# Kernel tuning notes

Measured on AMD Instinct MI355X. Metric: run time of the kernel, lower is better.

## Reference

```python
import jax, jax.numpy as jnp
import numpy as np

B = 8192
LOD = 60      # latent_obs_dim
LSD = 2 * LOD # latent state dim
AD = 10       # act_dim
NB = 15       # num_basis
BW = 3        # bandwidth
H = 60        # control-net hidden units


def elup1(x):
    # exp(x) if x < 0 else x + 1 (positive covariance activation)
    return jnp.where(x < 0.0, jnp.exp(x), x + 1.0)


def setup_inputs() -> dict:
    key = jax.random.key(0)
    ks = jax.random.split(key, 16)
    inp = {
        "post_mean": jax.random.normal(ks[0], (B, LSD), jnp.float32),
        "cu": jax.random.uniform(ks[1], (B, LOD), jnp.float32) + 0.1,
        "cl": jax.random.uniform(ks[2], (B, LOD), jnp.float32) + 0.1,
        "cs": 0.01 * jax.random.normal(ks[3], (B, LOD), jnp.float32),
        "action": jax.random.normal(ks[4], (B, AD), jnp.float32),
        # transition basis matrices (params); original init is zeros/+-0.2*I,
        # use small random values for a non-degenerate numerical test
        "tm11": 0.05 * jax.random.normal(ks[5], (NB, LOD, LOD), jnp.float32),
        "tm12": 0.2 * jnp.eye(LOD)[None] + 0.02 * jax.random.normal(ks[6], (NB, LOD, LOD), jnp.float32),
        "tm21": -0.2 * jnp.eye(LOD)[None] + 0.02 * jax.random.normal(ks[7], (NB, LOD, LOD), jnp.float32),
        "tm22": 0.05 * jax.random.normal(ks[8], (NB, LOD, LOD), jnp.float32),
        # log transition noise, init elup1_inv(1.0) = 0.0 -> perturb slightly
        "log_noise": 0.1 * jax.random.normal(ks[9], (1, LSD), jnp.float32),
        # coefficient net: Linear(LSD -> NB) + Softmax (no hidden layers)
        "w_coef": jax.random.normal(ks[10], (NB, LSD), jnp.float32) / np.sqrt(LSD),
        "b_coef": jnp.zeros((NB,), jnp.float32),
        # control net: Linear(AD -> H) + ReLU + Linear(H -> LSD)
        "w_c1": jax.random.normal(ks[11], (H, AD), jnp.float32) / np.sqrt(AD),
        "b_c1": jnp.zeros((H,), jnp.float32),
        "w_c2": jax.random.normal(ks[12], (LSD, H), jnp.float32) / np.sqrt(H),
        "b_c2": jnp.zeros((LSD,), jnp.float32),
    }
    return inp


def _band_mask():
    idx = jnp.arange(LOD)
    return (jnp.abs(idx[:, None] - idx[None, :]) <= BW).astype(jnp.float32)


def reference(post_mean, cu, cl, cs, action,
              tm11, tm12, tm21, tm22, log_noise,
              w_coef, b_coef, w_c1, b_c1, w_c2, b_c2):
    mask = _band_mask()            # [LOD, LOD]
    eye = jnp.eye(LOD, dtype=post_mean.dtype)

    # coefficient net + softmax -> basis-weighted transition matrices
    coef = jax.nn.softmax(post_mean @ w_coef.T + b_coef, axis=-1)  # [B, NB]

    def mix(tm):  # [B, LOD, LOD], band-masked
        return jnp.einsum('bk,kij->bij', coef, tm) * mask

    t11 = mix(tm11) + eye
    t12 = mix(tm12)
    t21 = mix(tm21)
    t22 = mix(tm22) + eye

    # control net contribution
    control = jax.nn.relu(action @ w_c1.T + b_c1) @ w_c2.T + b_c2  # [B, LSD]

    trans_cov = elup1(log_noise)        # [1, LSD]
    tc_u = trans_cov[..., :LOD]
    tc_l = trans_cov[..., LOD:]

    mu = post_mean[:, :LOD]
    ml = post_mean[:, LOD:]

    bmv = lambda m, v: jnp.einsum('bij,bj->bi', m, v)

    nmu = bmv(t11, mu) + bmv(t12, ml)
    nml = bmv(t21, mu) + bmv(t22, ml)

    # diagonal covariance predict (dadat / dadbt)
    ncu = bmv(t11 ** 2, cu) + 2.0 * bmv(t11 * t12, cs) + bmv(t12 ** 2, cl) + tc_u
    ncl = bmv(t21 ** 2, cu) + 2.0 * bmv(t21 * t22, cs) + bmv(t22 ** 2, cl) + tc_l
    ncs = bmv(t21 * t11, cu) + bmv(t22 * t11, cs) + bmv(t21 * t12, cs) + bmv(t22 * t12, cl)

    next_mean = jnp.concatenate([nmu, nml], axis=-1) + control
    return (next_mean, ncu, ncl, ncs)
```

## Files before the change

kernel.cpp:

```cpp
#include <hip/hip_runtime.h>
#include <math.h>

#define BATCH 8192
#define LOD 60
#define LSD 120
#define AD 10
#define NB 15
#define BW 3
#define H 60

#define NM_SZ (BATCH * LSD)
#define NC_SZ (BATCH * LOD)

#define RGS 8
#define RG_ROWS 8
#define NJJ 16
#define VSJ 65
#define VSV (NJJ * VSJ)
#define PACK_FLOATS (RG_ROWS * NB * 28)
#define VS_OFF PACK_FLOATS
#define VS_FLOATS (5 * VSV)
#define OVL_FLOATS (VS_OFF + VS_FLOATS)
#define COEF_OFF VS_OFF
#define HID_OFF (VS_OFF + NB * 64)
#define OST_PLANE (RG_ROWS * 65)

typedef float v2f __attribute__((ext_vector_type(2)));
#define FMA2(a, b, c) __builtin_elementwise_fma((a), (b), (c))

__device__ __forceinline__ float elup1f(float x) {
    return x < 0.0f ? __expf(x) : x + 1.0f;
}

__global__ __launch_bounds__(256, 4) void k_fused(
    const float* __restrict__ pm, const float* __restrict__ cu,
    const float* __restrict__ cl, const float* __restrict__ cs,
    const float* __restrict__ action,
    const float* __restrict__ tm11, const float* __restrict__ tm12,
    const float* __restrict__ tm21, const float* __restrict__ tm22,
    const float* __restrict__ log_noise,
    const float* __restrict__ w_coef, const float* __restrict__ b_coef,
    const float* __restrict__ w_c1, const float* __restrict__ b_c1,
    const float* __restrict__ w_c2, const float* __restrict__ b_c2,
    float* __restrict__ out)
{
    __shared__ __align__(16) float ovl[OVL_FLOATS];

    const int tid  = threadIdx.x;
    const int lane = tid & 63;
    const int wv   = __builtin_amdgcn_readfirstlane(tid >> 6);

    const int bid  = blockIdx.x;
    const int xcd  = bid & 7;
    const int slot = bid >> 3;
    const int bg   = xcd * 16 + (slot >> 3);
    const int rg   = slot & 7;
    const int b0   = bg * 64;
    const int i0   = rg * RG_ROWS;

    float* pack_s = ovl;
    float* vsb    = ovl + VS_OFF;
    float* coefL  = ovl + COEF_OFF;
    float* hid_s  = ovl + HID_OFF;

    {
        const int k0 = wv, k1 = wv + 4, k2 = wv + 8;
        const int k3 = (wv < 3) ? wv + 12 : 14;
        const float4* pmv = (const float4*)(pm + (size_t)(b0 + lane) * LSD);
        const float4* w0 = (const float4*)(w_coef + k0 * LSD);
        const float4* w1 = (const float4*)(w_coef + k1 * LSD);
        const float4* w2 = (const float4*)(w_coef + k2 * LSD);
        const float4* w3 = (const float4*)(w_coef + k3 * LSD);
        v2f a0 = {0.f, 0.f}, a1 = {0.f, 0.f}, a2 = {0.f, 0.f}, a3 = {0.f, 0.f};
        #pragma unroll 6
        for (int d = 0; d < LSD / 4; ++d) {
            float4 p = pmv[d];
            v2f plo = {p.x, p.y}, phi = {p.z, p.w};
            float4 u0 = w0[d], u1 = w1[d], u2 = w2[d], u3 = w3[d];
            a0 = FMA2(plo, ((v2f){u0.x, u0.y}), a0);
            a0 = FMA2(phi, ((v2f){u0.z, u0.w}), a0);
            a1 = FMA2(plo, ((v2f){u1.x, u1.y}), a1);
            a1 = FMA2(phi, ((v2f){u1.z, u1.w}), a1);
            a2 = FMA2(plo, ((v2f){u2.x, u2.y}), a2);
            a2 = FMA2(phi, ((v2f){u2.z, u2.w}), a2);
            a3 = FMA2(plo, ((v2f){u3.x, u3.y}), a3);
            a3 = FMA2(phi, ((v2f){u3.z, u3.w}), a3);
        }
        coefL[k0 * 64 + lane] = a0.x + a0.y + b_coef[k0];
        coefL[k1 * 64 + lane] = a1.x + a1.y + b_coef[k1];
        coefL[k2 * 64 + lane] = a2.x + a2.y + b_coef[k2];
        if (wv < 3) coefL[k3 * 64 + lane] = a3.x + a3.y + b_coef[k3];
    }
    {
        v2f av2[5];
        const float2* a2p = (const float2*)(action + (size_t)(b0 + lane) * AD);
        #pragma unroll
        for (int z = 0; z < 5; ++z) { float2 t2 = a2p[z]; av2[z] = (v2f){t2.x, t2.y}; }
        #pragma unroll
        for (int q = 0; q < 15; ++q) {
            int h = wv * 15 + q;
            v2f acc2 = {0.f, 0.f};
            #pragma unroll
            for (int z = 0; z < 5; ++z)
                acc2 = FMA2(av2[z], *(const v2f*)(w_c1 + h * AD + 2 * z), acc2);
            float acc = acc2.x + acc2.y + b_c1[h];
            hid_s[h * 65 + lane] = fmaxf(acc, 0.0f);
        }
    }
    __syncthreads();

    float vr[20];
    {
        const int jj  = tid & 15;
        const int j   = i0 - BW + jj;
        const bool jok = (j >= 0) && (j < LOD);
        #pragma unroll
        for (int z = 0; z < 20; ++z) {
            const int idx = z * 256 + tid;
            const int blc = (idx >> 4) & 63;
            const int bb  = b0 + blc;
            float val = 0.0f;
            if (jok) {
                const int v = z >> 2;
                if (v == 0)      val = pm[bb * LSD + j];
                else if (v == 1) val = pm[bb * LSD + LOD + j];
                else if (v == 2) val = cu[bb * LOD + j];
                else if (v == 3) val = cl[bb * LOD + j];
                else             val = cs[bb * LOD + j];
            }
            vr[z] = val;
        }
    }

    for (int idx = tid; idx < PACK_FLOATS; idx += 256) {
        int m  = idx & 3;
        int q  = idx >> 2;
        int jo = q % 7;
        int q2 = q / 7;
        int k  = q2 % NB;
        int ri = q2 / NB;
        int i  = i0 + ri;
        int j  = i - BW + jo;
        const float* tmm = (m == 0) ? tm11 : (m == 1) ? tm12 : (m == 2) ? tm21 : tm22;
        float val = (i < LOD && j >= 0 && j < LOD) ? tmm[k * (LOD * LOD) + i * LOD + j] : 0.0f;
        pack_s[idx] = val;
    }

    float cf[NB];
    {
        float mx = -1e30f;
        #pragma unroll
        for (int k = 0; k < NB; ++k) { cf[k] = coefL[k * 64 + lane]; mx = fmaxf(mx, cf[k]); }
        float sm = 0.0f;
        #pragma unroll
        for (int k = 0; k < NB; ++k) { cf[k] = __expf(cf[k] - mx); sm += cf[k]; }
        float inv = 1.0f / sm;
        #pragma unroll
        for (int k = 0; k < NB; ++k) cf[k] *= inv;
    }

    const int r0g = i0 + 2 * wv;
    const int c0  = (r0g < LOD) ? r0g : LOD - 1;
    const int c1  = (r0g + 1 < LOD) ? r0g + 1 : LOD - 1;
    float ctl0 = b_c2[c0], ctl1 = b_c2[c1];
    float ctl2 = b_c2[LOD + c0], ctl3 = b_c2[LOD + c1];
    #pragma unroll 4
    for (int h = 0; h < H; ++h) {
        float hv = hid_s[h * 65 + lane];
        ctl0 = fmaf(hv, w_c2[c0 * H + h], ctl0);
        ctl1 = fmaf(hv, w_c2[c1 * H + h], ctl1);
        ctl2 = fmaf(hv, w_c2[(LOD + c0) * H + h], ctl2);
        ctl3 = fmaf(hv, w_c2[(LOD + c1) * H + h], ctl3);
    }
    __syncthreads();

    {
        const int jj = tid & 15;
        #pragma unroll
        for (int z = 0; z < 20; ++z) {
            const int idx = z * 256 + tid;
            const int blc = (idx >> 4) & 63;
            vsb[(z >> 2) * VSV + jj * VSJ + blc] = vr[z];
        }
    }
    __syncthreads();

    float onm[2], onl[2], ouv[2], olv[2], osv[2];
    #pragma unroll
    for (int rr = 0; rr < 2; ++rr) {
        const int riu = 2 * wv + rr;
        const int iu  = i0 + riu;
        const int iuc = (iu < LOD) ? iu : LOD - 1;

        v2f t2[14];
        #pragma unroll
        for (int z = 0; z < 14; ++z) t2[z] = (v2f){0.f, 0.f};
        const float4* tp = (const float4*)pack_s + riu * (NB * 7);
        #pragma unroll
        for (int k = 0; k < NB; ++k) {
            v2f c2 = {cf[k], cf[k]};
            #pragma unroll
            for (int jo = 0; jo < 7; ++jo) {
                float4 tv = tp[k * 7 + jo];
                t2[2 * jo]     = FMA2(c2, ((v2f){tv.x, tv.y}), t2[2 * jo]);
                t2[2 * jo + 1] = FMA2(c2, ((v2f){tv.z, tv.w}), t2[2 * jo + 1]);
            }
        }
        t2[6].x += 1.0f;
        t2[7].y += 1.0f;

        v2f nm2  = {0.f, 0.f};
        v2f ncu2 = {0.f, 0.f};
        v2f ncl2 = {0.f, 0.f};
        v2f ncs2 = {0.f, 0.f};
        #pragma unroll
        for (int jo = 0; jo < 7; ++jo) {
            const int jj = riu + jo;
            float m_ = vsb[0 * VSV + jj * VSJ + lane];
            float n_ = vsb[1 * VSV + jj * VSJ + lane];
            float u_ = vsb[2 * VSV + jj * VSJ + lane];
            float l_ = vsb[3 * VSV + jj * VSJ + lane];
            float s_ = vsb[4 * VSV + jj * VSJ + lane];
            float A  = t2[2 * jo].x,     Bv = t2[2 * jo].y;
            float C  = t2[2 * jo + 1].x, D  = t2[2 * jo + 1].y;
            v2f AC = {A, C}, BD = {Bv, D}, AB = {A, Bv}, CD = {C, D};
            v2f us = {u_, s_}, sl = {s_, l_};
            nm2 = FMA2(AC, ((v2f){m_, m_}), nm2);
            nm2 = FMA2(BD, ((v2f){n_, n_}), nm2);
            v2f e = FMA2(((v2f){Bv, Bv}), sl, ((v2f){A, A}) * us);
            v2f f = FMA2(((v2f){D, D}),  sl, ((v2f){C, C}) * us);
            ncu2 = FMA2(AB, e, ncu2);
            ncl2 = FMA2(CD, f, ncl2);
            ncs2 = FMA2(CD, e, ncs2);
        }
        float nmu  = nm2.x + ((rr == 0) ? ctl0 : ctl1);
        float nml  = nm2.y + ((rr == 0) ? ctl2 : ctl3);
        float ncuv = ncu2.x + ncu2.y + elup1f(log_noise[iuc]);
        float nclv = ncl2.x + ncl2.y + elup1f(log_noise[LOD + iuc]);
        float ncsv = ncs2.x + ncs2.y;
        onm[rr] = nmu; onl[rr] = nml; ouv[rr] = ncuv; olv[rr] = nclv; osv[rr] = ncsv;
    }
    __syncthreads();

    float* ost = ovl;
    #pragma unroll
    for (int rr = 0; rr < 2; ++rr) {
        const int ri = 2 * wv + rr;
        ost[0 * OST_PLANE + ri * 65 + lane] = onm[rr];
        ost[1 * OST_PLANE + ri * 65 + lane] = onl[rr];
        ost[2 * OST_PLANE + ri * 65 + lane] = ouv[rr];
        ost[3 * OST_PLANE + ri * 65 + lane] = olv[rr];
        ost[4 * OST_PLANE + ri * 65 + lane] = osv[rr];
    }
    __syncthreads();

    for (int idx = tid; idx < 5 * 64 * 2; idx += 256) {
        int q   = idx & 1;
        int blc = (idx >> 1) & 63;
        int t5  = idx >> 7;
        if (i0 + q * 4 + 3 >= LOD) continue;
        int bb = b0 + blc;
        int ro = q * 4;
        float4 v;
        v.x = ost[t5 * OST_PLANE + (ro + 0) * 65 + blc];
        v.y = ost[t5 * OST_PLANE + (ro + 1) * 65 + blc];
        v.z = ost[t5 * OST_PLANE + (ro + 2) * 65 + blc];
        v.w = ost[t5 * OST_PLANE + (ro + 3) * 65 + blc];
        float* bp;
        if (t5 == 0)      bp = out + bb * LSD + i0;
        else if (t5 == 1) bp = out + bb * LSD + LOD + i0;
        else if (t5 == 2) bp = out + NM_SZ + bb * LOD + i0;
        else if (t5 == 3) bp = out + NM_SZ + NC_SZ + bb * LOD + i0;
        else              bp = out + NM_SZ + 2 * NC_SZ + bb * LOD + i0;
        *(float4*)(bp + ro) = v;
    }
}

extern "C" void kernel_launch(void* const* d_in, const int* in_sizes, int n_in,
                              void* d_out, int out_size, void* d_ws, size_t ws_size,
                              hipStream_t stream) {
    (void)in_sizes; (void)n_in; (void)out_size; (void)d_ws; (void)ws_size;
    const float* pm        = (const float*)d_in[0];
    const float* cu        = (const float*)d_in[1];
    const float* cl        = (const float*)d_in[2];
    const float* cs        = (const float*)d_in[3];
    const float* action    = (const float*)d_in[4];
    const float* tm11      = (const float*)d_in[5];
    const float* tm12      = (const float*)d_in[6];
    const float* tm21      = (const float*)d_in[7];
    const float* tm22      = (const float*)d_in[8];
    const float* log_noise = (const float*)d_in[9];
    const float* w_coef    = (const float*)d_in[10];
    const float* b_coef    = (const float*)d_in[11];
    const float* w_c1      = (const float*)d_in[12];
    const float* b_c1      = (const float*)d_in[13];
    const float* w_c2      = (const float*)d_in[14];
    const float* b_c2      = (const float*)d_in[15];

    hipLaunchKernelGGL(k_fused, dim3(1024), dim3(256), 0, stream,
                       pm, cu, cl, cs, action, tm11, tm12, tm21, tm22,
                       log_noise, w_coef, b_coef, w_c1, b_c1, w_c2, b_c2,
                       (float*)d_out);
}
```

Measured before the change: 117.7 us.

## Prepack banded transition matrices in a pre-kernel and read them from global memory

A new small kernel gathers the banded entries of the four transition basis matrices into a per-row packed workspace layout. The fused kernel then reads its mixing weights straight from that buffer with wave-uniform addresses, instead of having every block gather them into shared memory. This removes the per-block gather loop, shrinks the shared-memory footprint and drops two block barriers. The state vector loads are also issued earlier, and the covariance accumulation is rewritten as scalar FMAs. The cost is an extra kernel launch and a dependency on the workspace buffer.

```diff
diff --git a/kernel.cpp b/kernel.cpp
--- a/kernel.cpp
+++ b/kernel.cpp
@@ -12,36 +12,60 @@
 #define NM_SZ (BATCH * LSD)
 #define NC_SZ (BATCH * LOD)
 
+#define TMBG_STRIDE 448
+#define TMBG_ROW 420
+#define TMBG_FLOATS (LOD * TMBG_STRIDE)
+
 #define RGS 8
 #define RG_ROWS 8
 #define NJJ 16
 #define VSJ 65
 #define VSV (NJJ * VSJ)
-#define PACK_FLOATS (RG_ROWS * NB * 28)
-#define VS_OFF PACK_FLOATS
 #define VS_FLOATS (5 * VSV)
-#define OVL_FLOATS (VS_OFF + VS_FLOATS)
-#define COEF_OFF VS_OFF
-#define HID_OFF (VS_OFF + NB * 64)
+#define COEF_OFF VS_FLOATS
+#define HID_OFF (VS_FLOATS + NB * 64)
+#define OST_OFF VS_FLOATS
 #define OST_PLANE (RG_ROWS * 65)
+#define OVL_FLOATS (VS_FLOATS + 4860)
 
 typedef float v2f __attribute__((ext_vector_type(2)));
 #define FMA2(a, b, c) __builtin_elementwise_fma((a), (b), (c))
 
 __device__ __forceinline__ float elup1f(float x) {
     return x < 0.0f ? __expf(x) : x + 1.0f;
+}
+
+__global__ __launch_bounds__(256) void k_pack(
+    const float* __restrict__ tm11, const float* __restrict__ tm12,
+    const float* __restrict__ tm21, const float* __restrict__ tm22,
+    float* __restrict__ tmbg)
+{
+    int idx = blockIdx.x * 256 + threadIdx.x;
+    if (idx >= TMBG_FLOATS) return;
+    int i = idx / TMBG_STRIDE;
+    int r = idx - i * TMBG_STRIDE;
+    float val = 0.0f;
+    if (r < TMBG_ROW) {
+        int k  = r / 28;
+        int z  = r - k * 28;
+        int jo = z >> 2;
+        int m  = z & 3;
+        int j  = i - BW + jo;
+        const float* tmm = (m == 0) ? tm11 : (m == 1) ? tm12 : (m == 2) ? tm21 : tm22;
+        if (j >= 0 && j < LOD) val = tmm[k * (LOD * LOD) + i * LOD + j];
+    }
+    tmbg[idx] = val;
 }
 
 __global__ __launch_bounds__(256, 4) void k_fused(
     const float* __restrict__ pm, const float* __restrict__ cu,
     const float* __restrict__ cl, const float* __restrict__ cs,
     const float* __restrict__ action,
-    const float* __restrict__ tm11, const float* __restrict__ tm12,
-    const float* __restrict__ tm21, const float* __restrict__ tm22,
     const float* __restrict__ log_noise,
     const float* __restrict__ w_coef, const float* __restrict__ b_coef,
     const float* __restrict__ w_c1, const float* __restrict__ b_c1,
     const float* __restrict__ w_c2, const float* __restrict__ b_c2,
+    const float* __restrict__ tmbg,
     float* __restrict__ out)
 {
     __shared__ __align__(16) float ovl[OVL_FLOATS];
@@ -58,10 +82,32 @@
     const int b0   = bg * 64;
     const int i0   = rg * RG_ROWS;
 
-    float* pack_s = ovl;
-    float* vsb    = ovl + VS_OFF;
-    float* coefL  = ovl + COEF_OFF;
-    float* hid_s  = ovl + HID_OFF;
+    float* vsb   = ovl;
+    float* coefL = ovl + COEF_OFF;
+    float* hid_s = ovl + HID_OFF;
+
+    float vr[20];
+    {
+        const int jj  = tid & 15;
+        const int j   = i0 - BW + jj;
+        const bool jok = (j >= 0) && (j < LOD);
+        #pragma unroll
+        for (int z = 0; z < 20; ++z) {
+            const int idx = z * 256 + tid;
+            const int blc = (idx >> 4) & 63;
+            const int bb  = b0 + blc;
+            float val = 0.0f;
+            if (jok) {
+                const int v = z >> 2;
+                if (v == 0)      val = pm[bb * LSD + j];
+                else if (v == 1) val = pm[bb * LSD + LOD + j];
+                else if (v == 2) val = cu[bb * LOD + j];
+                else if (v == 3) val = cl[bb * LOD + j];
+                else             val = cs[bb * LOD + j];
+            }
+            vr[z] = val;
+        }
+    }
 
     {
         const int k0 = wv, k1 = wv + 4, k2 = wv + 8;
@@ -109,43 +155,6 @@
     }
     __syncthreads();
 
-    float vr[20];
-    {
-        const int jj  = tid & 15;
-        const int j   = i0 - BW + jj;
-        const bool jok = (j >= 0) && (j < LOD);
-        #pragma unroll
-        for (int z = 0; z < 20; ++z) {
-            const int idx = z * 256 + tid;
-            const int blc = (idx >> 4) & 63;
-            const int bb  = b0 + blc;
-            float val = 0.0f;
-            if (jok) {
-                const int v = z >> 2;
-                if (v == 0)      val = pm[bb * LSD + j];
-                else if (v == 1) val = pm[bb * LSD + LOD + j];
-                else if (v == 2) val = cu[bb * LOD + j];
-                else if (v == 3) val = cl[bb * LOD + j];
-                else             val = cs[bb * LOD + j];
-            }
-            vr[z] = val;
-        }
-    }
-
-    for (int idx = tid; idx < PACK_FLOATS; idx += 256) {
-        int m  = idx & 3;
-        int q  = idx >> 2;
-        int jo = q % 7;
-        int q2 = q / 7;
-        int k  = q2 % NB;
-        int ri = q2 / NB;
-        int i  = i0 + ri;
-        int j  = i - BW + jo;
-        const float* tmm = (m == 0) ? tm11 : (m == 1) ? tm12 : (m == 2) ? tm21 : tm22;
-        float val = (i < LOD && j >= 0 && j < LOD) ? tmm[k * (LOD * LOD) + i * LOD + j] : 0.0f;
-        pack_s[idx] = val;
-    }
-
     float cf[NB];
     {
         float mx = -1e30f;
@@ -158,7 +167,6 @@
         #pragma unroll
         for (int k = 0; k < NB; ++k) cf[k] *= inv;
     }
-
     const int r0g = i0 + 2 * wv;
     const int c0  = (r0g < LOD) ? r0g : LOD - 1;
     const int c1  = (r0g + 1 < LOD) ? r0g + 1 : LOD - 1;
@@ -172,7 +180,6 @@
         ctl2 = fmaf(hv, w_c2[(LOD + c0) * H + h], ctl2);
         ctl3 = fmaf(hv, w_c2[(LOD + c1) * H + h], ctl3);
     }
-    __syncthreads();
 
     {
         const int jj = tid & 15;
@@ -192,27 +199,25 @@
         const int iu  = i0 + riu;
         const int iuc = (iu < LOD) ? iu : LOD - 1;
 
+        const float* tpg = tmbg + (size_t)iuc * TMBG_STRIDE;
         v2f t2[14];
         #pragma unroll
         for (int z = 0; z < 14; ++z) t2[z] = (v2f){0.f, 0.f};
-        const float4* tp = (const float4*)pack_s + riu * (NB * 7);
         #pragma unroll
         for (int k = 0; k < NB; ++k) {
             v2f c2 = {cf[k], cf[k]};
             #pragma unroll
             for (int jo = 0; jo < 7; ++jo) {
-                float4 tv = tp[k * 7 + jo];
-                t2[2 * jo]     = FMA2(c2, ((v2f){tv.x, tv.y}), t2[2 * jo]);
-                t2[2 * jo + 1] = FMA2(c2, ((v2f){tv.z, tv.w}), t2[2 * jo + 1]);
+                v2f w01 = *(const v2f*)(tpg + k * 28 + jo * 4);
+                v2f w23 = *(const v2f*)(tpg + k * 28 + jo * 4 + 2);
+                t2[2 * jo]     = FMA2(c2, w01, t2[2 * jo]);
+                t2[2 * jo + 1] = FMA2(c2, w23, t2[2 * jo + 1]);
             }
         }
         t2[6].x += 1.0f;
         t2[7].y += 1.0f;
 
-        v2f nm2  = {0.f, 0.f};
-        v2f ncu2 = {0.f, 0.f};
-        v2f ncl2 = {0.f, 0.f};
-        v2f ncs2 = {0.f, 0.f};
+        float nmu = 0.f, nml = 0.f, ncuv = 0.f, nclv = 0.f, ncsv = 0.f;
         #pragma unroll
         for (int jo = 0; jo < 7; ++jo) {
             const int jj = riu + jo;
@@ -223,26 +228,24 @@
             float s_ = vsb[4 * VSV + jj * VSJ + lane];
             float A  = t2[2 * jo].x,     Bv = t2[2 * jo].y;
             float C  = t2[2 * jo + 1].x, D  = t2[2 * jo + 1].y;
-            v2f AC = {A, C}, BD = {Bv, D}, AB = {A, Bv}, CD = {C, D};
-            v2f us = {u_, s_}, sl = {s_, l_};
-            nm2 = FMA2(AC, ((v2f){m_, m_}), nm2);
-            nm2 = FMA2(BD, ((v2f){n_, n_}), nm2);
-            v2f e = FMA2(((v2f){Bv, Bv}), sl, ((v2f){A, A}) * us);
-            v2f f = FMA2(((v2f){D, D}),  sl, ((v2f){C, C}) * us);
-            ncu2 = FMA2(AB, e, ncu2);
-            ncl2 = FMA2(CD, f, ncl2);
-            ncs2 = FMA2(CD, e, ncs2);
-        }
-        float nmu  = nm2.x + ((rr == 0) ? ctl0 : ctl1);
-        float nml  = nm2.y + ((rr == 0) ? ctl2 : ctl3);
-        float ncuv = ncu2.x + ncu2.y + elup1f(log_noise[iuc]);
-        float nclv = ncl2.x + ncl2.y + elup1f(log_noise[LOD + iuc]);
-        float ncsv = ncs2.x + ncs2.y;
+            nmu = fmaf(A, m_, nmu);  nmu = fmaf(Bv, n_, nmu);
+            nml = fmaf(C, m_, nml);  nml = fmaf(D, n_, nml);
+            float e1 = fmaf(Bv, s_, A * u_);
+            float e2 = fmaf(Bv, l_, A * s_);
+            float f1 = fmaf(D, s_, C * u_);
+            float f2 = fmaf(D, l_, C * s_);
+            ncuv = fmaf(A, e1, ncuv);  ncuv = fmaf(Bv, e2, ncuv);
+            nclv = fmaf(C, f1, nclv);  nclv = fmaf(D, f2, nclv);
+            ncsv = fmaf(C, e1, ncsv);  ncsv = fmaf(D, e2, ncsv);
+        }
+        ncuv += elup1f(log_noise[iuc]);
+        nclv += elup1f(log_noise[LOD + iuc]);
+        nmu  += (rr == 0) ? ctl0 : ctl1;
+        nml  += (rr == 0) ? ctl2 : ctl3;
         onm[rr] = nmu; onl[rr] = nml; ouv[rr] = ncuv; olv[rr] = nclv; osv[rr] = ncsv;
     }
-    __syncthreads();
-
-    float* ost = ovl;
+
+    float* ost = ovl + OST_OFF;
     #pragma unroll
     for (int rr = 0; rr < 2; ++rr) {
         const int ri = 2 * wv + rr;
@@ -279,7 +282,7 @@
 extern "C" void kernel_launch(void* const* d_in, const int* in_sizes, int n_in,
                               void* d_out, int out_size, void* d_ws, size_t ws_size,
                               hipStream_t stream) {
-    (void)in_sizes; (void)n_in; (void)out_size; (void)d_ws; (void)ws_size;
+    (void)in_sizes; (void)n_in; (void)out_size; (void)ws_size;
     const float* pm        = (const float*)d_in[0];
     const float* cu        = (const float*)d_in[1];
     const float* cl        = (const float*)d_in[2];
@@ -297,8 +300,13 @@
     const float* w_c2      = (const float*)d_in[14];
     const float* b_c2      = (const float*)d_in[15];
 
+    float* tmbg = (float*)d_ws;
+
+    hipLaunchKernelGGL(k_pack, dim3((TMBG_FLOATS + 255) / 256), dim3(256), 0, stream,
+                       tm11, tm12, tm21, tm22, tmbg);
+
     hipLaunchKernelGGL(k_fused, dim3(1024), dim3(256), 0, stream,
-                       pm, cu, cl, cs, action, tm11, tm12, tm21, tm22,
-                       log_noise, w_coef, b_coef, w_c1, b_c1, w_c2, b_c2,
+                       pm, cu, cl, cs, action, log_noise,
+                       w_coef, b_coef, w_c1, b_c1, w_c2, b_c2, tmbg,
                        (float*)d_out);
 }
```

Result: no change. 116.6 us (median of 2 runs) (-0.9%).
